# Performance work log

Measured on AMD Instinct MI355X. Metric: run time of the kernel, lower is better.

Reference implementation:

```python
import jax, jax.numpy as jnp
import numpy as np

VOCAB, EMB, HID = 128, 512, 1024
B, T = 256, 256


def setup_inputs() -> dict:
    key = jax.random.key(0)
    ks = jax.random.split(key, 12)
    sc_e = 1.0 / np.sqrt(EMB)
    sc_h = 1.0 / np.sqrt(HID)
    u = lambda k, shape, s: jax.random.uniform(k, shape, jnp.float32, -s, s)
    return {
        "tokens": jax.random.randint(ks[0], (B, T), 0, VOCAB),
        "emb": jax.random.normal(ks[1], (VOCAB, EMB), jnp.float32),
        # layer 0: input size EMB
        "W_ih0": u(ks[2], (HID, EMB), sc_h), "W_hh0": u(ks[3], (HID, HID), sc_h),
        "b_ih0": u(ks[4], (HID,), sc_h), "b_hh0": u(ks[5], (HID,), sc_h),
        # layer 1: input size HID
        "W_ih1": u(ks[6], (HID, HID), sc_h), "W_hh1": u(ks[7], (HID, HID), sc_h),
        "b_ih1": u(ks[8], (HID,), sc_h), "b_hh1": u(ks[9], (HID,), sc_h),
        # output head
        "W_out": u(ks[10], (VOCAB, HID), sc_h), "b_out": u(ks[11], (VOCAB,), sc_h),
    }


def _rnn_layer(x, W_ih, W_hh, b_ih, b_hh):
    # x: [B, T, I] -> [B, T, H]; precompute the input projection as one big GEMM
    pre = jnp.einsum('bti,hi->bth', x, W_ih) + b_ih  # [B, T, H]
    h0 = jnp.zeros((x.shape[0], W_hh.shape[0]), x.dtype)

    def step(h, p):
        h = jnp.tanh(p + h @ W_hh.T + b_hh)
        return h, h

    _, ys = jax.lax.scan(step, h0, jnp.swapaxes(pre, 0, 1))  # ys: [T, B, H]
    return jnp.swapaxes(ys, 0, 1)


def reference(tokens, emb, W_ih0, W_hh0, b_ih0, b_hh0,
              W_ih1, W_hh1, b_ih1, b_hh1, W_out, b_out):
    x = emb[tokens]                                    # [B, T, EMB]
    x = _rnn_layer(x, W_ih0, W_hh0, b_ih0, b_hh0)      # [B, T, HID]
    x = _rnn_layer(x, W_ih1, W_hh1, b_ih1, b_hh1)      # [B, T, HID]
    return x[:, -1, :] @ W_out.T + b_out               # [B, VOCAB]
```

## Files before the change

### kernel.cpp

```cpp
#include <hip/hip_runtime.h>

typedef _Float16 f16x8 __attribute__((ext_vector_type(8)));
typedef float f32x4 __attribute__((ext_vector_type(4)));

#define VOCAB 128
#define EMB 512
#define HID 1024
#define BATCH 256
#define TSEQ 256
#define SLOT (BATCH * HID)

#define CTR0_B 0
#define CTRG_B 2048
#define CTR1_B 4096
#define H0_B   8192
#define H1_B   (H0_B + 4 * SLOT * 2)
#define PRE1_B (H1_B + 4 * SLOT * 2)
#define PROJ_B (PRE1_B + 4 * SLOT * 4)
#define WIMG_B (PROJ_B + VOCAB * HID * 4)

#define LOADX4(dst, p) asm volatile("global_load_dwordx4 %0, %1, off sc0 sc1" : "=v"(dst) : "v"(p))
#define LOADD(dst, p)  asm volatile("global_load_dword %0, %1, off sc0 sc1" : "=v"(dst) : "v"(p))
#define STOREX4(p, v)  asm volatile("global_store_dwordx4 %0, %1, off sc0 sc1" :: "v"(p), "v"(v) : "memory")
#define WAITV(n) do { asm volatile("s_waitcnt vmcnt(" #n ")" ::: "memory"); \
                      __builtin_amdgcn_sched_barrier(0); } while (0)

__device__ __forceinline__ f32x4 mfma16(f16x8 a, f16x8 b, f32x4 c) {
    return __builtin_amdgcn_mfma_f32_16x16x32_f16(a, b, c, 0, 0, 0);
}

__device__ __forceinline__ void spin32(unsigned int* p) {
    while (__hip_atomic_load(p, __ATOMIC_RELAXED, __HIP_MEMORY_SCOPE_AGENT) < 32u) {}
}

__global__ __launch_bounds__(256) void pack_w(const float* __restrict__ W,
                                              _Float16* __restrict__ img) {
    int i = blockIdx.x * 256 + threadIdx.x;
    if (i >= HID * 128) return;
    const int n = i >> 7;
    const int c = i & 127;
    const int cb = n >> 5;
    const int col = n & 31;
    const int nf = col >> 4, ar = col & 15;
    const int kc = c >> 2, g = c & 3;
    const float* src = W + (size_t)n * HID + c * 8;
    float4 u0 = *(const float4*)src;
    float4 u1 = *(const float4*)(src + 4);
    float uf[8] = {u0.x, u0.y, u0.z, u0.w, u1.x, u1.y, u1.z, u1.w};
    f16x8 hi, lo;
    #pragma unroll
    for (int j = 0; j < 8; ++j) {
        _Float16 h = (_Float16)uf[j];
        hi[j] = h;
        lo[j] = (_Float16)(uf[j] - (float)h);
    }
    const size_t base = (size_t)cb * 65536 + (size_t)kc * 2048 +
                        (size_t)nf * 512 + (size_t)g * 128 + (size_t)ar * 8;
    *(f16x8*)(img + base)        = hi;
    *(f16x8*)(img + base + 1024) = lo;
}

__global__ __launch_bounds__(256) void proj_k(const float* __restrict__ emb,
                                              const float* __restrict__ Wih0,
                                              const float* __restrict__ b_ih0,
                                              float* __restrict__ PROJ) {
    int o = blockIdx.x * 256 + threadIdx.x;
    if (o >= VOCAB * HID) return;
    const int v = o >> 10, n = o & (HID - 1);
    const float* er = emb + (size_t)v * EMB;
    const float* wr = Wih0 + (size_t)n * EMB;
    float acc = 0.f;
    #pragma unroll 4
    for (int k = 0; k < EMB; k += 4) {
        float4 e = *(const float4*)(er + k);
        float4 w = *(const float4*)(wr + k);
        acc += e.x * w.x + e.y * w.y + e.z * w.z + e.w * w.w;
    }
    PROJ[o] = acc + b_ih0[n];
}

#define ISSUE4(B0, B1, KCB) do { \
    const _Float16* q0_ = pr0 + (KCB) * 32; \
    const _Float16* q1_ = pr1 + (KCB) * 32; \
    LOADX4(B0[0], q0_);      LOADX4(B0[1], q0_ + 32); \
    LOADX4(B0[2], q0_ + 64); LOADX4(B0[3], q0_ + 96); \
    LOADX4(B1[0], q1_);      LOADX4(B1[1], q1_ + 32); \
    LOADX4(B1[2], q1_ + 64); LOADX4(B1[3], q1_ + 96); \
} while (0)

#define KC1(KC, AV0, AV1) do { \
    const _Float16* sb_ = simg + (KC) * 2048 + lane * 8; \
    f16x8 bh0_ = *(const f16x8*)sb_; \
    f16x8 bh1_ = *(const f16x8*)(sb_ + 512); \
    f16x8 bl0_ = *(const f16x8*)(sb_ + 1024); \
    f16x8 bl1_ = *(const f16x8*)(sb_ + 1536); \
    a00 = mfma16(AV0, bh0_, a00); a01 = mfma16(AV0, bh1_, a01); \
    a10 = mfma16(AV1, bh0_, a10); a11 = mfma16(AV1, bh1_, a11); \
    a00 = mfma16(AV0, bl0_, a00); a01 = mfma16(AV0, bl1_, a01); \
    a10 = mfma16(AV1, bl0_, a10); a11 = mfma16(AV1, bl1_, a11); \
} while (0)

#define KC4(KB, CB0, CB1) do { \
    KC1((KB) + 0, CB0[0], CB1[0]); \
    KC1((KB) + 1, CB0[1], CB1[1]); \
    KC1((KB) + 2, CB0[2], CB1[2]); \
    KC1((KB) + 3, CB0[3], CB1[3]); \
} while (0)

__global__ __launch_bounds__(256, 1) void rnn_run(
    const int* __restrict__ tokens,
    const float* __restrict__ b_hh0, const float* __restrict__ b_ih1,
    const float* __restrict__ b_hh1, char* __restrict__ ws)
{
    __shared__ _Float16 simg[65536];
    __shared__ __align__(16) char stageb[4][4096];

    _Float16* h0 = (_Float16*)(ws + H0_B);
    _Float16* h1 = (_Float16*)(ws + H1_B);
    float* pre1 = (float*)(ws + PRE1_B);
    const float* PROJ = (const float*)(ws + PROJ_B);
    const _Float16* wimg = (const _Float16*)(ws + WIMG_B);

    const int tid = threadIdx.x, lane = tid & 63, wv = tid >> 6;
    const int blk = blockIdx.x;
    const int role = blk >> 6;
    const int sub = blk & 63;
    const int cb = sub & 31, rg = sub >> 5;
    const int n0 = cb * 32;

    unsigned int* c0 = (unsigned int*)(ws + CTR0_B) + (rg << 8);
    unsigned int* cG = (unsigned int*)(ws + CTRG_B) + (rg << 8);
    unsigned int* c1 = (unsigned int*)(ws + CTR1_B) + (rg << 8);
    unsigned int* ctr_pub = (role == 0) ? c0 : (role == 1) ? cG : c1;

    {
        const _Float16* gi = wimg + (size_t)(role * 32 + cb) * 65536;
        for (int i = tid; i < 8192; i += 256)
            *(f16x8*)&simg[(size_t)i * 8] = *(const f16x8*)&gi[(size_t)i * 8];
    }
    __syncthreads();

    const int ar = lane & 15;
    const int g16 = lane >> 4;
    const int rbase = rg * 128 + wv * 32;
    const int er0 = rbase + g16 * 4;

    const float* bias = (role == 0) ? b_hh0 : (role == 1) ? b_ih1 : b_hh1;
    const float b0 = bias[n0 + ar];
    const float b1 = bias[n0 + 16 + ar];

    for (int st = 0; st < TSEQ; ++st) {
        if (lane == 0) {
            if (role == 0) {
                if (st) spin32(c0 + st - 1);
            } else if (role == 1) {
                spin32(c0 + st);
            } else {
                spin32(cG + st);
                if (st) spin32(c1 + st - 1);
            }
        }

        const _Float16* A = (role == 0) ? h0 + (size_t)((st + 3) & 3) * SLOT
                          : (role == 1) ? h0 + (size_t)(st & 3) * SLOT
                                        : h1 + (size_t)((st + 3) & 3) * SLOT;
        const _Float16* pr0 = A + (size_t)(rbase + ar) * HID + g16 * 8;
        const _Float16* pr1 = pr0 + 16 * HID;

        f32x4 a00 = {}, a01 = {}, a10 = {}, a11 = {};
        f16x8 cA0[4], cA1[4], cB0[4], cB1[4], cC0[4], cC1[4], cD0[4], cD1[4];
        float pv0[8], pv1[8];

        __builtin_amdgcn_sched_barrier(0);
        if (role == 2) {
            const float* P = pre1 + (size_t)(st & 3) * SLOT;
            #pragma unroll
            for (int mf = 0; mf < 2; ++mf) {
                #pragma unroll
                for (int r = 0; r < 4; ++r) {
                    const int rr = er0 + mf * 16 + r;
                    LOADD(pv0[mf * 4 + r], P + (size_t)rr * HID + n0 + ar);
                    LOADD(pv1[mf * 4 + r], P + (size_t)rr * HID + n0 + 16 + ar);
                }
            }
        }
        ISSUE4(cA0, cA1, 0);
        ISSUE4(cB0, cB1, 4);
        ISSUE4(cC0, cC1, 8);
        ISSUE4(cD0, cD1, 12);
        WAITV(24); KC4(0,  cA0, cA1); ISSUE4(cA0, cA1, 16);
        WAITV(24); KC4(4,  cB0, cB1); ISSUE4(cB0, cB1, 20);
        WAITV(24); KC4(8,  cC0, cC1); ISSUE4(cC0, cC1, 24);
        WAITV(24); KC4(12, cD0, cD1); ISSUE4(cD0, cD1, 28);
        WAITV(24); KC4(16, cA0, cA1);
        WAITV(16); KC4(20, cB0, cB1);
        WAITV(8);  KC4(24, cC0, cC1);
        WAITV(0);  KC4(28, cD0, cD1);
        __builtin_amdgcn_sched_barrier(0);

        if (lane == 0) {
            if (role == 0) {
                if (st >= 4) spin32(cG + st - 4);
            } else if (role == 1) {
                if (st >= 4) spin32(c1 + st - 4);
            }
        }

        if (role == 0) {
            _Float16* sg = (_Float16*)stageb[wv];
            _Float16* O = h0 + (size_t)(st & 3) * SLOT;
            #pragma unroll
            for (int mf = 0; mf < 2; ++mf) {
                #pragma unroll
                for (int r = 0; r < 4; ++r) {
                    const int rr = er0 + mf * 16 + r;
                    const int trow = g16 * 4 + mf * 16 + r;
                    const int tok = tokens[rr * TSEQ + st];
                    const float* pr = PROJ + (size_t)tok * HID + n0;
                    const float v0 = (mf ? a10[r] : a00[r]) + pr[ar] + b0;
                    const float v1 = (mf ? a11[r] : a01[r]) + pr[16 + ar] + b1;
                    sg[trow * 32 + ar]      = (_Float16)tanhf(v0);
                    sg[trow * 32 + 16 + ar] = (_Float16)tanhf(v1);
                }
            }
            __syncthreads();
            #pragma unroll
            for (int j = 0; j < 2; ++j) {
                const int trow = j * 16 + (lane >> 2);
                f32x4 sv = *(const f32x4*)((const char*)sg + trow * 64 + (lane & 3) * 16);
                STOREX4(O + (size_t)(rbase + trow) * HID + n0 + (lane & 3) * 8, sv);
            }
        } else if (role == 1) {
            float* sg = (float*)stageb[wv];
            float* O = pre1 + (size_t)(st & 3) * SLOT;
            #pragma unroll
            for (int mf = 0; mf < 2; ++mf) {
                #pragma unroll
                for (int r = 0; r < 4; ++r) {
                    const int trow = g16 * 4 + mf * 16 + r;
                    sg[trow * 32 + ar]      = (mf ? a10[r] : a00[r]) + b0;
                    sg[trow * 32 + 16 + ar] = (mf ? a11[r] : a01[r]) + b1;
                }
            }
            __syncthreads();
            #pragma unroll
            for (int i = 0; i < 4; ++i) {
                const int trow = i * 8 + (lane >> 3);
                f32x4 sv = *(const f32x4*)((const char*)sg + trow * 128 + (lane & 7) * 16);
                STOREX4(O + (size_t)(rbase + trow) * HID + n0 + (lane & 7) * 4, sv);
            }
        } else {
            _Float16* sg = (_Float16*)stageb[wv];
            _Float16* O = h1 + (size_t)(st & 3) * SLOT;
            #pragma unroll
            for (int mf = 0; mf < 2; ++mf) {
                #pragma unroll
                for (int r = 0; r < 4; ++r) {
                    const int trow = g16 * 4 + mf * 16 + r;
                    const float v0 = (mf ? a10[r] : a00[r]) + pv0[mf * 4 + r] + b0;
                    const float v1 = (mf ? a11[r] : a01[r]) + pv1[mf * 4 + r] + b1;
                    sg[trow * 32 + ar]      = (_Float16)tanhf(v0);
                    sg[trow * 32 + 16 + ar] = (_Float16)tanhf(v1);
                }
            }
            __syncthreads();
            #pragma unroll
            for (int j = 0; j < 2; ++j) {
                const int trow = j * 16 + (lane >> 2);
                f32x4 sv = *(const f32x4*)((const char*)sg + trow * 64 + (lane & 3) * 16);
                STOREX4(O + (size_t)(rbase + trow) * HID + n0 + (lane & 3) * 8, sv);
            }
        }

        asm volatile("s_waitcnt vmcnt(0)" ::: "memory");
        __syncthreads();
        if (tid == 0)
            __hip_atomic_fetch_add(ctr_pub + st, 1u, __ATOMIC_RELAXED,
                                   __HIP_MEMORY_SCOPE_AGENT);
    }
}

__global__ __launch_bounds__(256) void head2(const _Float16* __restrict__ h1last,
                                             const float* __restrict__ Wout,
                                             const float* __restrict__ b_out,
                                             float* __restrict__ out) {
    const int idx = blockIdx.x * 256 + threadIdx.x;
    const int m = idx >> 7, n = idx & 127;
    const _Float16* hr = h1last + (size_t)m * HID;
    const float* wr = Wout + (size_t)n * HID;
    float acc = 0.f;
    #pragma unroll 4
    for (int k = 0; k < HID; k += 8) {
        f16x8 hv = *(const f16x8*)(hr + k);
        float4 w0 = *(const float4*)(wr + k);
        float4 w1 = *(const float4*)(wr + k + 4);
        acc += (float)hv[0] * w0.x + (float)hv[1] * w0.y +
               (float)hv[2] * w0.z + (float)hv[3] * w0.w +
               (float)hv[4] * w1.x + (float)hv[5] * w1.y +
               (float)hv[6] * w1.z + (float)hv[7] * w1.w;
    }
    out[idx] = acc + b_out[n];
}

extern "C" void kernel_launch(void* const* d_in, const int* in_sizes, int n_in,
                              void* d_out, int out_size, void* d_ws, size_t ws_size,
                              hipStream_t stream) {
    const int*   tokens = (const int*)  d_in[0];
    const float* emb    = (const float*)d_in[1];
    const float* W_ih0  = (const float*)d_in[2];
    const float* W_hh0  = (const float*)d_in[3];
    const float* b_ih0  = (const float*)d_in[4];
    const float* b_hh0  = (const float*)d_in[5];
    const float* W_ih1  = (const float*)d_in[6];
    const float* W_hh1  = (const float*)d_in[7];
    const float* b_ih1  = (const float*)d_in[8];
    const float* b_hh1  = (const float*)d_in[9];
    const float* W_out  = (const float*)d_in[10];
    const float* b_out  = (const float*)d_in[11];
    float* out = (float*)d_out;

    char* ws = (char*)d_ws;
    _Float16* wimg = (_Float16*)(ws + WIMG_B);
    float* PROJ = (float*)(ws + PROJ_B);

    (void)hipMemsetAsync(ws + CTR0_B, 0, 8192, stream);
    (void)hipMemsetAsync(ws + H0_B + (size_t)3 * SLOT * 2, 0, (size_t)SLOT * 2, stream);
    (void)hipMemsetAsync(ws + H1_B + (size_t)3 * SLOT * 2, 0, (size_t)SLOT * 2, stream);

    pack_w<<<512, 256, 0, stream>>>(W_hh0, wimg);
    pack_w<<<512, 256, 0, stream>>>(W_ih1, wimg + (size_t)32 * 65536);
    pack_w<<<512, 256, 0, stream>>>(W_hh1, wimg + (size_t)64 * 65536);
    proj_k<<<512, 256, 0, stream>>>(emb, W_ih0, b_ih0, PROJ);

    rnn_run<<<192, 256, 0, stream>>>(tokens, b_hh0, b_ih1, b_hh1, ws);

    head2<<<128, 256, 0, stream>>>((const _Float16*)(ws + H1_B) + (size_t)3 * SLOT,
                                   W_out, b_out, out);
}
```

Measured before the change: 4.264 ms.

## Drop fp16 hi/lo weight split and widen blocks to 64 columns

Recurrent and input weights are packed as a single fp16 image instead of fp16 hi plus fp16 residual lo. The freed shared memory holds 64 output columns per block, so the persistent kernel runs 96 blocks and waits for 16 arrivals per counter instead of 32. This halves the MFMA count per output and the number of blocks in each barrier. In exchange, the weights lose roughly 11 bits of effective precision, which across 256 recurrent steps may push the output past tolerance. The pre1 loads in role 2 also move from before the GEMM to after it, so they are no longer overlapped.

```diff
diff --git a/kernel.cpp b/kernel.cpp
--- a/kernel.cpp
+++ b/kernel.cpp
@@ -29,8 +29,8 @@
     return __builtin_amdgcn_mfma_f32_16x16x32_f16(a, b, c, 0, 0, 0);
 }
 
-__device__ __forceinline__ void spin32(unsigned int* p) {
-    while (__hip_atomic_load(p, __ATOMIC_RELAXED, __HIP_MEMORY_SCOPE_AGENT) < 32u) {}
+__device__ __forceinline__ void spin16(unsigned int* p) {
+    while (__hip_atomic_load(p, __ATOMIC_RELAXED, __HIP_MEMORY_SCOPE_AGENT) < 16u) {}
 }
 
 __global__ __launch_bounds__(256) void pack_w(const float* __restrict__ W,
@@ -39,25 +39,20 @@
     if (i >= HID * 128) return;
     const int n = i >> 7;
     const int c = i & 127;
-    const int cb = n >> 5;
-    const int col = n & 31;
-    const int nf = col >> 4, ar = col & 15;
+    const int cb = n >> 6;
+    const int nf = (n >> 4) & 3, ar = n & 15;
     const int kc = c >> 2, g = c & 3;
     const float* src = W + (size_t)n * HID + c * 8;
     float4 u0 = *(const float4*)src;
     float4 u1 = *(const float4*)(src + 4);
-    float uf[8] = {u0.x, u0.y, u0.z, u0.w, u1.x, u1.y, u1.z, u1.w};
-    f16x8 hi, lo;
-    #pragma unroll
-    for (int j = 0; j < 8; ++j) {
-        _Float16 h = (_Float16)uf[j];
-        hi[j] = h;
-        lo[j] = (_Float16)(uf[j] - (float)h);
-    }
+    f16x8 hv;
+    hv[0] = (_Float16)u0.x; hv[1] = (_Float16)u0.y;
+    hv[2] = (_Float16)u0.z; hv[3] = (_Float16)u0.w;
+    hv[4] = (_Float16)u1.x; hv[5] = (_Float16)u1.y;
+    hv[6] = (_Float16)u1.z; hv[7] = (_Float16)u1.w;
     const size_t base = (size_t)cb * 65536 + (size_t)kc * 2048 +
                         (size_t)nf * 512 + (size_t)g * 128 + (size_t)ar * 8;
-    *(f16x8*)(img + base)        = hi;
-    *(f16x8*)(img + base + 1024) = lo;
+    *(f16x8*)(img + base) = hv;
 }
 
 __global__ __launch_bounds__(256) void proj_k(const float* __restrict__ emb,
@@ -90,14 +85,14 @@
 
 #define KC1(KC, AV0, AV1) do { \
     const _Float16* sb_ = simg + (KC) * 2048 + lane * 8; \
-    f16x8 bh0_ = *(const f16x8*)sb_; \
-    f16x8 bh1_ = *(const f16x8*)(sb_ + 512); \
-    f16x8 bl0_ = *(const f16x8*)(sb_ + 1024); \
-    f16x8 bl1_ = *(const f16x8*)(sb_ + 1536); \
-    a00 = mfma16(AV0, bh0_, a00); a01 = mfma16(AV0, bh1_, a01); \
-    a10 = mfma16(AV1, bh0_, a10); a11 = mfma16(AV1, bh1_, a11); \
-    a00 = mfma16(AV0, bl0_, a00); a01 = mfma16(AV0, bl1_, a01); \
-    a10 = mfma16(AV1, bl0_, a10); a11 = mfma16(AV1, bl1_, a11); \
+    f16x8 b0_ = *(const f16x8*)sb_; \
+    f16x8 b1_ = *(const f16x8*)(sb_ + 512); \
+    f16x8 b2_ = *(const f16x8*)(sb_ + 1024); \
+    f16x8 b3_ = *(const f16x8*)(sb_ + 1536); \
+    a00 = mfma16(AV0, b0_, a00); a01 = mfma16(AV0, b1_, a01); \
+    a02 = mfma16(AV0, b2_, a02); a03 = mfma16(AV0, b3_, a03); \
+    a10 = mfma16(AV1, b0_, a10); a11 = mfma16(AV1, b1_, a11); \
+    a12 = mfma16(AV1, b2_, a12); a13 = mfma16(AV1, b3_, a13); \
 } while (0)
 
 #define KC4(KB, CB0, CB1) do { \
@@ -123,10 +118,10 @@
 
     const int tid = threadIdx.x, lane = tid & 63, wv = tid >> 6;
     const int blk = blockIdx.x;
-    const int role = blk >> 6;
-    const int sub = blk & 63;
-    const int cb = sub & 31, rg = sub >> 5;
-    const int n0 = cb * 32;
+    const int role = blk >> 5;
+    const int sub = blk & 31;
+    const int cb = sub & 15, rg = sub >> 4;
+    const int n0 = cb * 64;
 
     unsigned int* c0 = (unsigned int*)(ws + CTR0_B) + (rg << 8);
     unsigned int* cG = (unsigned int*)(ws + CTRG_B) + (rg << 8);
@@ -134,7 +129,7 @@
     unsigned int* ctr_pub = (role == 0) ? c0 : (role == 1) ? cG : c1;
 
     {
-        const _Float16* gi = wimg + (size_t)(role * 32 + cb) * 65536;
+        const _Float16* gi = wimg + (size_t)(role * 16 + cb) * 65536;
         for (int i = tid; i < 8192; i += 256)
             *(f16x8*)&simg[(size_t)i * 8] = *(const f16x8*)&gi[(size_t)i * 8];
     }
@@ -146,18 +141,20 @@
     const int er0 = rbase + g16 * 4;
 
     const float* bias = (role == 0) ? b_hh0 : (role == 1) ? b_ih1 : b_hh1;
-    const float b0 = bias[n0 + ar];
-    const float b1 = bias[n0 + 16 + ar];
+    const float bb0 = bias[n0 + ar];
+    const float bb1 = bias[n0 + 16 + ar];
+    const float bb2 = bias[n0 + 32 + ar];
+    const float bb3 = bias[n0 + 48 + ar];
 
     for (int st = 0; st < TSEQ; ++st) {
         if (lane == 0) {
             if (role == 0) {
-                if (st) spin32(c0 + st - 1);
+                if (st) spin16(c0 + st - 1);
             } else if (role == 1) {
-                spin32(c0 + st);
+                spin16(c0 + st);
             } else {
-                spin32(cG + st);
-                if (st) spin32(c1 + st - 1);
+                spin16(cG + st);
+                if (st) spin16(c1 + st - 1);
             }
         }
 
@@ -167,23 +164,11 @@
         const _Float16* pr0 = A + (size_t)(rbase + ar) * HID + g16 * 8;
         const _Float16* pr1 = pr0 + 16 * HID;
 
-        f32x4 a00 = {}, a01 = {}, a10 = {}, a11 = {};
+        f32x4 a00 = {}, a01 = {}, a02 = {}, a03 = {};
+        f32x4 a10 = {}, a11 = {}, a12 = {}, a13 = {};
         f16x8 cA0[4], cA1[4], cB0[4], cB1[4], cC0[4], cC1[4], cD0[4], cD1[4];
-        float pv0[8], pv1[8];
 
         __builtin_amdgcn_sched_barrier(0);
-        if (role == 2) {
-            const float* P = pre1 + (size_t)(st & 3) * SLOT;
-            #pragma unroll
-            for (int mf = 0; mf < 2; ++mf) {
-                #pragma unroll
-                for (int r = 0; r < 4; ++r) {
-                    const int rr = er0 + mf * 16 + r;
-                    LOADD(pv0[mf * 4 + r], P + (size_t)rr * HID + n0 + ar);
-                    LOADD(pv1[mf * 4 + r], P + (size_t)rr * HID + n0 + 16 + ar);
-                }
-            }
-        }
         ISSUE4(cA0, cA1, 0);
         ISSUE4(cB0, cB1, 4);
         ISSUE4(cC0, cC1, 8);
@@ -200,9 +185,9 @@
 
         if (lane == 0) {
             if (role == 0) {
-                if (st >= 4) spin32(cG + st - 4);
+                if (st >= 4) spin16(cG + st - 4);
             } else if (role == 1) {
-                if (st >= 4) spin32(c1 + st - 4);
+                if (st >= 4) spin16(c1 + st - 4);
             }
         }
 
@@ -210,65 +195,114 @@
             _Float16* sg = (_Float16*)stageb[wv];
             _Float16* O = h0 + (size_t)(st & 3) * SLOT;
             #pragma unroll
-            for (int mf = 0; mf < 2; ++mf) {
-                #pragma unroll
-                for (int r = 0; r < 4; ++r) {
-                    const int rr = er0 + mf * 16 + r;
-                    const int trow = g16 * 4 + mf * 16 + r;
-                    const int tok = tokens[rr * TSEQ + st];
-                    const float* pr = PROJ + (size_t)tok * HID + n0;
-                    const float v0 = (mf ? a10[r] : a00[r]) + pr[ar] + b0;
-                    const float v1 = (mf ? a11[r] : a01[r]) + pr[16 + ar] + b1;
-                    sg[trow * 32 + ar]      = (_Float16)tanhf(v0);
-                    sg[trow * 32 + 16 + ar] = (_Float16)tanhf(v1);
-                }
+            for (int r = 0; r < 4; ++r) {
+                const int rr = er0 + r;
+                const int trow = g16 * 4 + r;
+                const int tok = tokens[rr * TSEQ + st];
+                const float* pr = PROJ + (size_t)tok * HID + n0;
+                sg[trow * 64 +      ar] = (_Float16)tanhf(a00[r] + pr[ar]      + bb0);
+                sg[trow * 64 + 16 + ar] = (_Float16)tanhf(a01[r] + pr[16 + ar] + bb1);
+                sg[trow * 64 + 32 + ar] = (_Float16)tanhf(a02[r] + pr[32 + ar] + bb2);
+                sg[trow * 64 + 48 + ar] = (_Float16)tanhf(a03[r] + pr[48 + ar] + bb3);
+            }
+            #pragma unroll
+            for (int r = 0; r < 4; ++r) {
+                const int rr = er0 + 16 + r;
+                const int trow = 16 + g16 * 4 + r;
+                const int tok = tokens[rr * TSEQ + st];
+                const float* pr = PROJ + (size_t)tok * HID + n0;
+                sg[trow * 64 +      ar] = (_Float16)tanhf(a10[r] + pr[ar]      + bb0);
+                sg[trow * 64 + 16 + ar] = (_Float16)tanhf(a11[r] + pr[16 + ar] + bb1);
+                sg[trow * 64 + 32 + ar] = (_Float16)tanhf(a12[r] + pr[32 + ar] + bb2);
+                sg[trow * 64 + 48 + ar] = (_Float16)tanhf(a13[r] + pr[48 + ar] + bb3);
             }
             __syncthreads();
             #pragma unroll
-            for (int j = 0; j < 2; ++j) {
-                const int trow = j * 16 + (lane >> 2);
-                f32x4 sv = *(const f32x4*)((const char*)sg + trow * 64 + (lane & 3) * 16);
-                STOREX4(O + (size_t)(rbase + trow) * HID + n0 + (lane & 3) * 8, sv);
+            for (int j = 0; j < 4; ++j) {
+                const int c = j * 64 + lane;
+                const int row = c >> 3, part = c & 7;
+                f32x4 sv = *(const f32x4*)((const char*)sg + row * 128 + part * 16);
+                STOREX4(O + (size_t)(rbase + row) * HID + n0 + part * 8, sv);
             }
         } else if (role == 1) {
-            float* sg = (float*)stageb[wv];
+            float* sgf = (float*)stageb[wv];
             float* O = pre1 + (size_t)(st & 3) * SLOT;
             #pragma unroll
-            for (int mf = 0; mf < 2; ++mf) {
-                #pragma unroll
-                for (int r = 0; r < 4; ++r) {
-                    const int trow = g16 * 4 + mf * 16 + r;
-                    sg[trow * 32 + ar]      = (mf ? a10[r] : a00[r]) + b0;
-                    sg[trow * 32 + 16 + ar] = (mf ? a11[r] : a01[r]) + b1;
-                }
-            }
-            __syncthreads();
-            #pragma unroll
-            for (int i = 0; i < 4; ++i) {
-                const int trow = i * 8 + (lane >> 3);
-                f32x4 sv = *(const f32x4*)((const char*)sg + trow * 128 + (lane & 7) * 16);
-                STOREX4(O + (size_t)(rbase + trow) * HID + n0 + (lane & 7) * 4, sv);
+            for (int r = 0; r < 4; ++r) {
+                const int t0 = g16 * 4 + r, t1 = 16 + g16 * 4 + r;
+                sgf[t0 * 32 + ar]      = a00[r] + bb0;
+                sgf[t0 * 32 + 16 + ar] = a01[r] + bb1;
+                sgf[t1 * 32 + ar]      = a10[r] + bb0;
+                sgf[t1 * 32 + 16 + ar] = a11[r] + bb1;
+            }
+            #pragma unroll
+            for (int j = 0; j < 4; ++j) {
+                const int c = j * 64 + lane;
+                const int row = c >> 3, part = c & 7;
+                f32x4 sv = *(const f32x4*)((const char*)sgf + row * 128 + part * 16);
+                STOREX4(O + (size_t)(rbase + row) * HID + n0 + part * 4, sv);
+            }
+            #pragma unroll
+            for (int r = 0; r < 4; ++r) {
+                const int t0 = g16 * 4 + r, t1 = 16 + g16 * 4 + r;
+                sgf[t0 * 32 + ar]      = a02[r] + bb2;
+                sgf[t0 * 32 + 16 + ar] = a03[r] + bb3;
+                sgf[t1 * 32 + ar]      = a12[r] + bb2;
+                sgf[t1 * 32 + 16 + ar] = a13[r] + bb3;
+            }
+            #pragma unroll
+            for (int j = 0; j < 4; ++j) {
+                const int c = j * 64 + lane;
+                const int row = c >> 3, part = c & 7;
+                f32x4 sv = *(const f32x4*)((const char*)sgf + row * 128 + part * 16);
+                STOREX4(O + (size_t)(rbase + row) * HID + n0 + 32 + part * 4, sv);
             }
         } else {
+            const float* P = pre1 + (size_t)(st & 3) * SLOT;
+            float pv00[4], pv01[4], pv02[4], pv03[4];
+            float pv10[4], pv11[4], pv12[4], pv13[4];
+            #pragma unroll
+            for (int r = 0; r < 4; ++r) {
+                const size_t o0 = (size_t)(er0 + r) * HID + n0 + ar;
+                LOADD(pv00[r], P + o0);
+                LOADD(pv01[r], P + o0 + 16);
+                LOADD(pv02[r], P + o0 + 32);
+                LOADD(pv03[r], P + o0 + 48);
+            }
+            #pragma unroll
+            for (int r = 0; r < 4; ++r) {
+                const size_t o1 = (size_t)(er0 + 16 + r) * HID + n0 + ar;
+                LOADD(pv10[r], P + o1);
+                LOADD(pv11[r], P + o1 + 16);
+                LOADD(pv12[r], P + o1 + 32);
+                LOADD(pv13[r], P + o1 + 48);
+            }
+            WAITV(0);
             _Float16* sg = (_Float16*)stageb[wv];
             _Float16* O = h1 + (size_t)(st & 3) * SLOT;
             #pragma unroll
-            for (int mf = 0; mf < 2; ++mf) {
-                #pragma unroll
-                for (int r = 0; r < 4; ++r) {
-                    const int trow = g16 * 4 + mf * 16 + r;
-                    const float v0 = (mf ? a10[r] : a00[r]) + pv0[mf * 4 + r] + b0;
-                    const float v1 = (mf ? a11[r] : a01[r]) + pv1[mf * 4 + r] + b1;
-                    sg[trow * 32 + ar]      = (_Float16)tanhf(v0);
-                    sg[trow * 32 + 16 + ar] = (_Float16)tanhf(v1);
-                }
+            for (int r = 0; r < 4; ++r) {
+                const int trow = g16 * 4 + r;
+                sg[trow * 64 +      ar] = (_Float16)tanhf(a00[r] + pv00[r] + bb0);
+                sg[trow * 64 + 16 + ar] = (_Float16)tanhf(a01[r] + pv01[r] + bb1);
+                sg[trow * 64 + 32 + ar] = (_Float16)tanhf(a02[r] + pv02[r] + bb2);
+                sg[trow * 64 + 48 + ar] = (_Float16)tanhf(a03[r] + pv03[r] + bb3);
+            }
+            #pragma unroll
+            for (int r = 0; r < 4; ++r) {
+                const int trow = 16 + g16 * 4 + r;
+                sg[trow * 64 +      ar] = (_Float16)tanhf(a10[r] + pv10[r] + bb0);
+                sg[trow * 64 + 16 + ar] = (_Float16)tanhf(a11[r] + pv11[r] + bb1);
+                sg[trow * 64 + 32 + ar] = (_Float16)tanhf(a12[r] + pv12[r] + bb2);
+                sg[trow * 64 + 48 + ar] = (_Float16)tanhf(a13[r] + pv13[r] + bb3);
             }
             __syncthreads();
             #pragma unroll
-            for (int j = 0; j < 2; ++j) {
-                const int trow = j * 16 + (lane >> 2);
-                f32x4 sv = *(const f32x4*)((const char*)sg + trow * 64 + (lane & 3) * 16);
-                STOREX4(O + (size_t)(rbase + trow) * HID + n0 + (lane & 3) * 8, sv);
+            for (int j = 0; j < 4; ++j) {
+                const int c = j * 64 + lane;
+                const int row = c >> 3, part = c & 7;
+                f32x4 sv = *(const f32x4*)((const char*)sg + row * 128 + part * 16);
+                STOREX4(O + (size_t)(rbase + row) * HID + n0 + part * 8, sv);
             }
         }
 
@@ -328,11 +362,11 @@
     (void)hipMemsetAsync(ws + H1_B + (size_t)3 * SLOT * 2, 0, (size_t)SLOT * 2, stream);
 
     pack_w<<<512, 256, 0, stream>>>(W_hh0, wimg);
-    pack_w<<<512, 256, 0, stream>>>(W_ih1, wimg + (size_t)32 * 65536);
-    pack_w<<<512, 256, 0, stream>>>(W_hh1, wimg + (size_t)64 * 65536);
+    pack_w<<<512, 256, 0, stream>>>(W_ih1, wimg + (size_t)16 * 65536);
+    pack_w<<<512, 256, 0, stream>>>(W_hh1, wimg + (size_t)32 * 65536);
     proj_k<<<512, 256, 0, stream>>>(emb, W_ih0, b_ih0, PROJ);
 
-    rnn_run<<<192, 256, 0, stream>>>(tokens, b_hh0, b_ih1, b_hh1, ws);
+    rnn_run<<<96, 256, 0, stream>>>(tokens, b_hh0, b_ih1, b_hh1, ws);
 
     head2<<<128, 256, 0, stream>>>((const _Float16*)(ws + H1_B) + (size_t)3 * SLOT,
                                    W_out, b_out, out);
```

Result: slower. 4.577 ms (+7.3%).
